# Kernel tuning notes

Hardware: AMD Instinct MI355X
Metric: run time of the kernel (lower is better)

Reference implementation:

```python
import jax, jax.numpy as jnp
import numpy as np

B, S, HOPS, DIM, NREL = 1024, 32, 2, 64, 237
NENT, NEDGE = 14541, 272115
SIGMA = 0.1
CFMW = 64


def setup_inputs() -> dict:
    key = jax.random.key(0)
    ks = jax.random.split(key, 20)

    def g(k, shape):
        return (jax.random.normal(k, shape, dtype=jnp.float32) / np.float32(np.sqrt(shape[0])))

    inp = {
        "entity_pairs": jax.random.randint(ks[0], (B, 2), 0, NENT),
        "train_edges": jax.random.randint(ks[1], (B,), 0, NEDGE),
        "labels": jax.random.randint(ks[2], (B,), 0, NREL),
        "entity2edges": jax.random.randint(ks[3], (NENT + 1, S), 0, NEDGE + 1),
        "edge2entities": jax.random.randint(ks[4], (NEDGE + 1, 1), 0, NENT + 1),
        "edge2relation": jax.random.randint(ks[5], (NEDGE + 1,), 0, NREL + 1),
        "t": jax.random.uniform(ks[6], (B,), dtype=jnp.float32),
        "eps": jax.random.normal(ks[7], (B, NREL), dtype=jnp.float32),
        "rel_feat": g(ks[8], (NREL, DIM)),
        "W_agg0": g(ks[9], (DIM, DIM)), "b_agg0": jnp.zeros((DIM,), jnp.float32),
        "W_agg1": g(ks[10], (DIM, NREL)), "b_agg1": jnp.zeros((NREL,), jnp.float32),
        "W_out": g(ks[11], (2 * NREL, NREL)), "b_out": jnp.zeros((NREL,), jnp.float32),
        "mW1": g(ks[12], (NREL + 1, CFMW)), "mb1": jnp.zeros((CFMW,), jnp.float32),
        "mW2": g(ks[13], (CFMW, CFMW)), "mb2": jnp.zeros((CFMW,), jnp.float32),
        "mW3": g(ks[14], (CFMW, CFMW)), "mb3": jnp.zeros((CFMW,), jnp.float32),
        "mW4": g(ks[15], (CFMW, NREL)), "mb4": jnp.zeros((NREL,), jnp.float32),
    }
    return inp


def _side(ent, labels, train_edges, entity2edges, edge2entities, edge2relation, relf, aggs):
    # multi-hop neighbor edge gather + masks (exclude the training edge itself)
    edges_list = [labels]  # hop-0 "edges" are the relation labels
    masks = []
    for i in range(HOPS):
        if i == 0:
            ne = ent.reshape(B, 1)  # (B, 1) source entities
        else:
            ne = edge2entities[edges_list[-1].reshape(-1)].reshape(B, -1)
        nedges = entity2edges[ne.reshape(-1)].reshape(B, -1)  # (B, S**(i+1))
        edges_list.append(nedges)
        masks.append((nedges != train_edges[:, None]).astype(relf.dtype))
    # edge -> relation -> feature
    ev = [relf[edges_list[0]]]  # (B, DIM)
    for edges in edges_list[1:]:
        ev.append(relf[edge2relation[edges]])  # (B, S**h, DIM)
    # iterative mean aggregation (PathCon-style, one entity per edge)
    for i in range(HOPS):
        W, b, act, self_inc = aggs[i]
        d = W.shape[0]
        nxt = []
        for hop in range(HOPS - i):
            neigh = ev[hop + 1].reshape(B, -1, 1, S, d)
            m = masks[hop].reshape(B, -1, 1, S, 1)
            out = jnp.mean(jnp.mean(neigh * m, axis=-2), axis=-2)  # (B, S**hop, d)
            if self_inc:
                out = out + ev[hop].reshape(B, -1, d)
            nxt.append(act(out @ W + b))
        ev = nxt
    return ev[0].reshape(B, NREL)


def reference(entity_pairs, train_edges, labels, entity2edges, edge2entities,
              edge2relation, t, eps, rel_feat, W_agg0, b_agg0, W_agg1, b_agg1,
              W_out, b_out, mW1, mb1, mW2, mb2, mW3, mb3, mW4, mb4):
    relf = jnp.concatenate([rel_feat, jnp.zeros((1, DIM), rel_feat.dtype)], axis=0)
    aggs = [
        (W_agg0, b_agg0, jax.nn.relu, True),    # intermediate hop: relu, self-included
        (W_agg1, b_agg1, lambda x: x, False),   # last hop: identity, no self
    ]
    x0 = _side(entity_pairs[:, 0], labels, train_edges, entity2edges,
               edge2entities, edge2relation, relf, aggs)
    x1 = _side(entity_pairs[:, 1], labels, train_edges, entity2edges,
               edge2entities, edge2relation, relf, aggs)
    output = jnp.concatenate([x0, x1], axis=-1) @ W_out + b_out  # (B, NREL)
    # CFM: xt = (1-t) x0 + t x1 + sigma*eps ; ut = x1 - x0
    tb = t[:, None]
    xt = (1.0 - tb) * x0 + tb * x1 + SIGMA * eps
    h = jnp.concatenate([xt, tb], axis=-1)
    h = jax.nn.selu(h @ mW1 + mb1)
    h = jax.nn.selu(h @ mW2 + mb2)
    h = jax.nn.selu(h @ mW3 + mb3)
    vt = h @ mW4 + mb4
    scores = output * vt
    return scores
```

## Files before the change

kernel.cpp:

```cpp
#include <hip/hip_runtime.h>
#include <math.h>

#define BB 1024
#define S 32
#define DIM 64
#define NREL 237
#define SIGMA 0.1f

#define OFS_WR    0
#define N_WR      (238*64)
#define OFS_WC0   (OFS_WR + N_WR)
#define N_WC      (64*237)
#define OFS_WC1   (OFS_WC0 + N_WC)
#define OFS_BC    (OFS_WC1 + N_WC)
#define OFS_HC    (OFS_BC + 237)

__device__ __forceinline__ float selu_f(float x) {
    const float alpha = 1.6732632423543772f;
    const float scale = 1.0507009873554805f;
    return scale * (x > 0.f ? x : alpha * expm1f(x));
}

__global__ __launch_bounds__(256) void precompute_kernel(
    const float* __restrict__ rel_feat, const float* __restrict__ W0,
    const float* __restrict__ W1, const float* __restrict__ b1,
    const float* __restrict__ W_out, const float* __restrict__ b_out,
    const float* __restrict__ mW1, const float* __restrict__ mb1,
    float* __restrict__ ws) {
    __shared__ float red[256];
    int blk = blockIdx.x;
    const int tid = threadIdx.x;

    if (blk < 60) {
        int idx = blk * 256 + tid;
        if (idx < 238 * 64) {
            int r = idx >> 6, o = idx & 63;
            float acc = 0.f;
            if (r < NREL) {
#pragma unroll 8
                for (int d = 0; d < 64; ++d)
                    acc += rel_feat[r * 64 + d] * W0[d * 64 + o];
            }
            ws[OFS_WR + idx] = acc;
        }
        return;
    }
    blk -= 60;
    if (blk < 512) {
        int half = blk >> 8;
        int lb = blk & 255;
        int o = lb >> 2, ct = lb & 3;
        int cl = tid & 63, g = tid >> 6;
        int c = ct * 64 + cl;
        const float* Wsrc = W_out + half * 237 * 237;
        float acc = 0.f;
        if (c < NREL) {
            int k0 = g * 60, k1 = (g == 3) ? 237 : (k0 + 60);
#pragma unroll 4
            for (int k = k0; k < k1; ++k)
                acc += W1[o * 237 + k] * Wsrc[k * 237 + c];
        }
        red[tid] = acc;
        __syncthreads();
        if (g == 0 && c < NREL) {
            float s = red[cl] + red[64 + cl] + red[128 + cl] + red[192 + cl];
            ws[(half ? OFS_WC1 : OFS_WC0) + o * 237 + c] = s;
        }
        return;
    }
    blk -= 512;
    if (blk < 4) {
        int cl = tid & 63, g = tid >> 6;
        int c = blk * 64 + cl;
        float acc = 0.f;
        if (c < NREL) {
            int k0 = g * 60, k1 = (g == 3) ? 237 : (k0 + 60);
#pragma unroll 4
            for (int k = k0; k < k1; ++k)
                acc += b1[k] * (W_out[k * 237 + c] + W_out[(237 + k) * 237 + c]);
        }
        red[tid] = acc;
        __syncthreads();
        if (g == 0 && c < NREL)
            ws[OFS_BC + c] = b_out[c] + red[cl] + red[64 + cl] + red[128 + cl] + red[192 + cl];
        return;
    }
    {
        int w = tid & 63, g = tid >> 6;
        int k0 = g * 60, k1 = (g == 3) ? 237 : (k0 + 60);
        float acc = 0.f;
#pragma unroll 4
        for (int k = k0; k < k1; ++k)
            acc += b1[k] * mW1[k * 64 + w];
        red[tid] = acc;
        __syncthreads();
        if (g == 0)
            ws[OFS_HC + w] = mb1[w] + red[w] + red[64 + w] + red[128 + w] + red[192 + w];
    }
}

__global__ __launch_bounds__(256) void gf_kernel(
    const int* __restrict__ ep, const int* __restrict__ te_arr,
    const int* __restrict__ e2e_tab, const int* __restrict__ e2ent,
    const int* __restrict__ e2r, const float* __restrict__ b0,
    const float* __restrict__ t_arr, const float* __restrict__ eps,
    const float* __restrict__ W1, const float* __restrict__ mW1,
    const float* __restrict__ mW2, const float* __restrict__ mb2,
    const float* __restrict__ mW3, const float* __restrict__ mb3,
    const float* __restrict__ mW4, const float* __restrict__ mb4,
    const float* __restrict__ ws, float* __restrict__ out) {
    extern __shared__ float smem[];
    float* s_wr   = smem;
    int*   s_r2m  = (int*)(smem + 15232);
    int*   s_r1   = (int*)(smem + 16256);
    int*   s_ent2 = (int*)(smem + 16384);
    float* s_m1   = smem + 16512;
    float* s_v1   = smem + 16640;
    float* s_ov   = smem + 18816;

    const int tid = threadIdx.x;
    const int bb = blockIdx.x * 2;
    const int g = tid >> 4;
    const int c = tid & 15;
    const int te0 = te_arr[bb];
    const int te1 = te_arr[bb + 1];
    const float4 b0v = ((const float4*)b0)[c];

    {
        const float4* src = (const float4*)(ws + OFS_WR);
        float4* dst = (float4*)s_wr;
        for (int i = tid; i < 238 * 16; i += 256) dst[i] = src[i];
    }
    const float4* sWr4 = (const float4*)s_wr;

    if (tid < 128) {
        int u = tid >> 5, s = tid & 31;
        int b = bb + (u >> 1), side = u & 1;
        int te = (u >> 1) ? te1 : te0;
        int ent = ep[b * 2 + side];
        int e1 = e2e_tab[ent * S + s];
        s_r1[u * 32 + s] = e2r[e1];
        s_m1[u * 32 + s] = (e1 != te) ? 1.0f : 0.0f;
        s_ent2[u * 32 + s] = e2ent[e1];
    }
    __syncthreads();

    {
        const int te = te0;
        for (int p = tid; p < 1024; p += 256) {
            int j = p >> 5, s = p & 31;
            int e2 = e2e_tab[s_ent2[j] * S + s];
            s_r2m[p] = (e2 == te) ? NREL : e2r[e2];
        }
    }
    __syncthreads();

    for (int u = 0; u < 4; ++u) {
        for (int jj = g; jj < 32; jj += 16) {
            float4 acc = sWr4[s_r1[u * 32 + jj] * 16 + c];
            float4 sa = make_float4(0.f, 0.f, 0.f, 0.f);
            float4 sb = make_float4(0.f, 0.f, 0.f, 0.f);
            const int* rr = &s_r2m[jj * 32];
#pragma unroll
            for (int s = 0; s < 16; ++s) {
                float4 v = sWr4[rr[s] * 16 + c];
                sa.x += v.x; sa.y += v.y; sa.z += v.z; sa.w += v.w;
            }
#pragma unroll
            for (int s = 16; s < 32; ++s) {
                float4 v = sWr4[rr[s] * 16 + c];
                sb.x += v.x; sb.y += v.y; sb.z += v.z; sb.w += v.w;
            }
            const float inv = 1.0f / 32.0f;
            float m = s_m1[u * 32 + jj];
            float4 r;
            r.x = fmaxf(acc.x + (sa.x + sb.x) * inv + b0v.x, 0.f) * m;
            r.y = fmaxf(acc.y + (sa.y + sb.y) * inv + b0v.y, 0.f) * m;
            r.z = fmaxf(acc.z + (sa.z + sb.z) * inv + b0v.z, 0.f) * m;
            r.w = fmaxf(acc.w + (sa.w + sb.w) * inv + b0v.w, 0.f) * m;
            *((float4*)&s_v1[jj * 68 + c * 4]) = r;
        }
        __syncthreads();
        if (tid < 64) {
            float sum = 0.f;
#pragma unroll 8
            for (int j = 0; j < 32; ++j) sum += s_v1[j * 68 + tid];
            s_ov[u * 64 + tid] = sum * (1.0f / 32.0f);
        }
        if (u < 3) {
            const int un = u + 1;
            const int te = (un >> 1) ? te1 : te0;
            for (int p = tid; p < 1024; p += 256) {
                int j = p >> 5, s = p & 31;
                int e2 = e2e_tab[s_ent2[un * 32 + j] * S + s];
                s_r2m[p] = (e2 == te) ? NREL : e2r[e2];
            }
        }
        __syncthreads();
    }

    float* s_omix = smem;
    float* s_ymix = smem + 128;
    float* s_out  = smem + 608;
    float* s_red  = smem + 1088;
    float* s_h    = smem + 1600;
    const float tb0v = t_arr[bb];
    const float tb1v = t_arr[bb + 1];
    const float* Wc0 = ws + OFS_WC0;
    const float* Wc1 = ws + OFS_WC1;
    const float* bc = ws + OFS_BC;
    const float* hc = ws + OFS_HC;

    if (tid < 128) {
        int p = tid >> 6, w = tid & 63;
        float tb = p ? tb1v : tb0v;
        float o0 = s_ov[(p * 2 + 0) * 64 + w];
        float o1 = s_ov[(p * 2 + 1) * 64 + w];
        s_omix[p * 64 + w] = (1.f - tb) * o0 + tb * o1;
    }
    __syncthreads();

    if (tid < NREL) {
        float y0 = 0.f, y1 = 0.f;
#pragma unroll 4
        for (int d = 0; d < 64; ++d) {
            float w1v = W1[d * 237 + tid];
            y0 += s_omix[d] * w1v;
            y1 += s_omix[64 + d] * w1v;
        }
        s_ymix[tid] = y0;
        s_ymix[240 + tid] = y1;
        float a0 = bc[tid], a1 = a0;
#pragma unroll 4
        for (int d = 0; d < 64; ++d) {
            float w0 = Wc0[d * 237 + tid];
            float w1 = Wc1[d * 237 + tid];
            a0 += s_ov[d] * w0 + s_ov[64 + d] * w1;
            a1 += s_ov[128 + d] * w0 + s_ov[192 + d] * w1;
        }
        s_out[tid] = a0;
        s_out[240 + tid] = a1;
    }
    __syncthreads();

    {
        int w = tid & 63, gg = tid >> 6;
        float a0 = 0.f, a1 = 0.f;
        int k0 = gg * 60, k1 = (gg == 3) ? 237 : (k0 + 60);
        const float* e0 = eps + bb * 237;
        const float* e1 = eps + (bb + 1) * 237;
#pragma unroll 4
        for (int k = k0; k < k1; ++k) {
            float m = mW1[k * 64 + w];
            a0 += (SIGMA * e0[k] + s_ymix[k]) * m;
            a1 += (SIGMA * e1[k] + s_ymix[240 + k]) * m;
        }
        s_red[tid] = a0;
        s_red[256 + tid] = a1;
    }
    __syncthreads();
    if (tid < 128) {
        int p = tid >> 6, w = tid & 63;
        float tb = p ? tb1v : tb0v;
        float h = hc[w] + tb * mW1[237 * 64 + w]
                + s_red[p * 256 + w] + s_red[p * 256 + 64 + w]
                + s_red[p * 256 + 128 + w] + s_red[p * 256 + 192 + w];
        s_h[p * 64 + w] = selu_f(h);
    }
    __syncthreads();

    {
        int w = tid & 63, gg = tid >> 6;
        float a0 = 0.f, a1 = 0.f;
#pragma unroll
        for (int d = gg * 16; d < gg * 16 + 16; ++d) {
            float m = mW2[d * 64 + w];
            a0 += s_h[d] * m;
            a1 += s_h[64 + d] * m;
        }
        s_red[tid] = a0;
        s_red[256 + tid] = a1;
    }
    __syncthreads();
    if (tid < 128) {
        int p = tid >> 6, w = tid & 63;
        float v = mb2[w] + s_red[p * 256 + w] + s_red[p * 256 + 64 + w]
                + s_red[p * 256 + 128 + w] + s_red[p * 256 + 192 + w];
        s_h[p * 64 + w] = selu_f(v);
    }
    __syncthreads();

    {
        int w = tid & 63, gg = tid >> 6;
        float a0 = 0.f, a1 = 0.f;
#pragma unroll
        for (int d = gg * 16; d < gg * 16 + 16; ++d) {
            float m = mW3[d * 64 + w];
            a0 += s_h[d] * m;
            a1 += s_h[64 + d] * m;
        }
        s_red[tid] = a0;
        s_red[256 + tid] = a1;
    }
    __syncthreads();
    if (tid < 128) {
        int p = tid >> 6, w = tid & 63;
        float v = mb3[w] + s_red[p * 256 + w] + s_red[p * 256 + 64 + w]
                + s_red[p * 256 + 128 + w] + s_red[p * 256 + 192 + w];
        s_h[p * 64 + w] = selu_f(v);
    }
    __syncthreads();

    if (tid < NREL) {
        float a0 = mb4[tid], a1 = a0;
#pragma unroll 4
        for (int w = 0; w < 64; ++w) {
            float m = mW4[w * 237 + tid];
            a0 += s_h[w] * m;
            a1 += s_h[64 + w] * m;
        }
        out[bb * 237 + tid] = s_out[tid] * a0;
        out[(bb + 1) * 237 + tid] = s_out[240 + tid] * a1;
    }
}

extern "C" void kernel_launch(void* const* d_in, const int* in_sizes, int n_in,
                              void* d_out, int out_size, void* d_ws, size_t ws_size,
                              hipStream_t stream) {
    const int* ep       = (const int*)d_in[0];
    const int* te       = (const int*)d_in[1];
    const int* e2e      = (const int*)d_in[3];
    const int* e2ent    = (const int*)d_in[4];
    const int* e2r      = (const int*)d_in[5];
    const float* t      = (const float*)d_in[6];
    const float* eps    = (const float*)d_in[7];
    const float* relf   = (const float*)d_in[8];
    const float* W0     = (const float*)d_in[9];
    const float* b0     = (const float*)d_in[10];
    const float* W1     = (const float*)d_in[11];
    const float* b1     = (const float*)d_in[12];
    const float* W_out  = (const float*)d_in[13];
    const float* b_out  = (const float*)d_in[14];
    const float* mW1    = (const float*)d_in[15];
    const float* mb1    = (const float*)d_in[16];
    const float* mW2    = (const float*)d_in[17];
    const float* mb2    = (const float*)d_in[18];
    const float* mW3    = (const float*)d_in[19];
    const float* mb3    = (const float*)d_in[20];
    const float* mW4    = (const float*)d_in[21];
    const float* mb4    = (const float*)d_in[22];
    float* ws  = (float*)d_ws;
    float* out = (float*)d_out;

    hipLaunchKernelGGL(precompute_kernel, dim3(577), dim3(256), 0, stream,
                       relf, W0, W1, b1, W_out, b_out, mW1, mb1, ws);
    hipLaunchKernelGGL(gf_kernel, dim3(BB / 2), dim3(256), 76288, stream,
                       ep, te, e2e, e2ent, e2r, b0,
                       t, eps, W1, mW1, mW2, mb2, mW3, mb3, mW4, mb4, ws, out);
}
```

Measured before the change: 156.5 us.

## Pre-reduce hop-1 rows in registers to shrink LDS and fit two blocks per CU

Each thread now handles both of its hop-1 rows (g and g+16) in one interleaved gather loop and sums the two ReLU outputs in registers. It writes only 16 partial rows to shared memory instead of 32, which shrinks the dynamic LDS allocation from 76288 to 71936 bytes. A launch bound of 2 blocks per CU is added, aiming to let two 256-thread blocks share a CU's LDS and to interleave independent gathers for more ILP. The risks are higher register pressure from the two accumulator sets and a final reduction order that differs slightly. Whether two blocks actually fit depends on the other shared arrays used later in the kernel.

```diff
diff --git a/kernel.cpp b/kernel.cpp
--- a/kernel.cpp
+++ b/kernel.cpp
@@ -14,6 +14,8 @@
 #define OFS_WC1   (OFS_WC0 + N_WC)
 #define OFS_BC    (OFS_WC1 + N_WC)
 #define OFS_HC    (OFS_BC + 237)
+
+#define LDS_BYTES 71936
 
 __device__ __forceinline__ float selu_f(float x) {
     const float alpha = 1.6732632423543772f;
@@ -99,7 +101,7 @@
     }
 }
 
-__global__ __launch_bounds__(256) void gf_kernel(
+__global__ __launch_bounds__(256, 2) void gf_kernel(
     const int* __restrict__ ep, const int* __restrict__ te_arr,
     const int* __restrict__ e2e_tab, const int* __restrict__ e2ent,
     const int* __restrict__ e2r, const float* __restrict__ b0,
@@ -110,13 +112,13 @@
     const float* __restrict__ mW4, const float* __restrict__ mb4,
     const float* __restrict__ ws, float* __restrict__ out) {
     extern __shared__ float smem[];
-    float* s_wr   = smem;
-    int*   s_r2m  = (int*)(smem + 15232);
-    int*   s_r1   = (int*)(smem + 16256);
-    int*   s_ent2 = (int*)(smem + 16384);
-    float* s_m1   = smem + 16512;
-    float* s_v1   = smem + 16640;
-    float* s_ov   = smem + 18816;
+    float* s_wr      = smem;
+    int*   s_r2m     = (int*)(smem + 15232);
+    int*   s_r1      = (int*)(smem + 16256);
+    int*   s_ent2    = (int*)(smem + 16384);
+    float* s_m1      = smem + 16512;
+    float* s_partial = smem + 16640;
+    float* s_ov      = smem + 17728;
 
     const int tid = threadIdx.x;
     const int bb = blockIdx.x * 2;
@@ -156,35 +158,38 @@
     __syncthreads();
 
     for (int u = 0; u < 4; ++u) {
-        for (int jj = g; jj < 32; jj += 16) {
-            float4 acc = sWr4[s_r1[u * 32 + jj] * 16 + c];
-            float4 sa = make_float4(0.f, 0.f, 0.f, 0.f);
-            float4 sb = make_float4(0.f, 0.f, 0.f, 0.f);
-            const int* rr = &s_r2m[jj * 32];
+        const int jA = g, jB = g + 16;
+        const int* rrA = &s_r2m[jA * 32];
+        const int* rrB = &s_r2m[jB * 32];
+        float4 aA = sWr4[s_r1[u * 32 + jA] * 16 + c];
+        float4 aB = sWr4[s_r1[u * 32 + jB] * 16 + c];
+        float4 sA = make_float4(0.f, 0.f, 0.f, 0.f);
+        float4 sB = make_float4(0.f, 0.f, 0.f, 0.f);
 #pragma unroll
-            for (int s = 0; s < 16; ++s) {
-                float4 v = sWr4[rr[s] * 16 + c];
-                sa.x += v.x; sa.y += v.y; sa.z += v.z; sa.w += v.w;
-            }
-#pragma unroll
-            for (int s = 16; s < 32; ++s) {
-                float4 v = sWr4[rr[s] * 16 + c];
-                sb.x += v.x; sb.y += v.y; sb.z += v.z; sb.w += v.w;
-            }
-            const float inv = 1.0f / 32.0f;
-            float m = s_m1[u * 32 + jj];
-            float4 r;
-            r.x = fmaxf(acc.x + (sa.x + sb.x) * inv + b0v.x, 0.f) * m;
-            r.y = fmaxf(acc.y + (sa.y + sb.y) * inv + b0v.y, 0.f) * m;
-            r.z = fmaxf(acc.z + (sa.z + sb.z) * inv + b0v.z, 0.f) * m;
-            r.w = fmaxf(acc.w + (sa.w + sb.w) * inv + b0v.w, 0.f) * m;
-            *((float4*)&s_v1[jj * 68 + c * 4]) = r;
-        }
+        for (int s = 0; s < 32; ++s) {
+            float4 vA = sWr4[rrA[s] * 16 + c];
+            float4 vB = sWr4[rrB[s] * 16 + c];
+            sA.x += vA.x; sA.y += vA.y; sA.z += vA.z; sA.w += vA.w;
+            sB.x += vB.x; sB.y += vB.y; sB.z += vB.z; sB.w += vB.w;
+        }
+        const float inv = 1.0f / 32.0f;
+        float mA = s_m1[u * 32 + jA];
+        float mB = s_m1[u * 32 + jB];
+        float4 r;
+        r.x = fmaxf(aA.x + sA.x * inv + b0v.x, 0.f) * mA
+            + fmaxf(aB.x + sB.x * inv + b0v.x, 0.f) * mB;
+        r.y = fmaxf(aA.y + sA.y * inv + b0v.y, 0.f) * mA
+            + fmaxf(aB.y + sB.y * inv + b0v.y, 0.f) * mB;
+        r.z = fmaxf(aA.z + sA.z * inv + b0v.z, 0.f) * mA
+            + fmaxf(aB.z + sB.z * inv + b0v.z, 0.f) * mB;
+        r.w = fmaxf(aA.w + sA.w * inv + b0v.w, 0.f) * mA
+            + fmaxf(aB.w + sB.w * inv + b0v.w, 0.f) * mB;
+        *((float4*)&s_partial[g * 68 + c * 4]) = r;
         __syncthreads();
         if (tid < 64) {
             float sum = 0.f;
-#pragma unroll 8
-            for (int j = 0; j < 32; ++j) sum += s_v1[j * 68 + tid];
+#pragma unroll
+            for (int j = 0; j < 16; ++j) sum += s_partial[j * 68 + tid];
             s_ov[u * 64 + tid] = sum * (1.0f / 32.0f);
         }
         if (u < 3) {
@@ -354,7 +359,7 @@
 
     hipLaunchKernelGGL(precompute_kernel, dim3(577), dim3(256), 0, stream,
                        relf, W0, W1, b1, W_out, b_out, mW1, mb1, ws);
-    hipLaunchKernelGGL(gf_kernel, dim3(BB / 2), dim3(256), 76288, stream,
+    hipLaunchKernelGGL(gf_kernel, dim3(BB / 2), dim3(256), LDS_BYTES, stream,
                        ep, te, e2e, e2ent, e2r, b0,
                        t, eps, W1, mW1, mW2, mb2, mW3, mb3, mW4, mb4, ws, out);
 }
```

Result: no change. 157.4 us (+0.6%).
